# Kernel optimization log

Hardware: AMD Instinct MI355X
Metric: run time of the kernel (lower is better)

The kernel has to match this reference:

```python
import jax, jax.numpy as jnp
import numpy as np

N_ENT, N_REL, E_DIM, R_DIM, K, B = 100000, 64, 128, 128, 32, 16384


def _lookup_maxnorm(table, ids):
    # torch nn.Embedding(max_norm=1): rows with L2 norm > 1 are renormed to 1 at lookup
    x = table[ids]
    n = jnp.linalg.norm(x, axis=-1, keepdims=True)
    return x * jnp.minimum(1.0, 1.0 / jnp.maximum(n, 1e-12))


def setup_inputs() -> dict:
    key = jax.random.key(0)
    ks = jax.random.split(key, 10)
    xavier = lambda k, shp: jax.random.uniform(k, shp, jnp.float32, -1.0, 1.0) * np.sqrt(6.0 / (shp[0] + shp[1]))
    return {
        "idx": jax.random.randint(ks[0], (B,), 0, N_ENT),
        "adj_ent": jax.random.randint(ks[1], (N_ENT, K), 0, N_ENT),
        "adj_rel": jax.random.randint(ks[2], (N_ENT, K), 0, N_REL),
        "ent_table": xavier(ks[3], (N_ENT, E_DIM)),
        "rel_table": xavier(ks[4], (N_REL, R_DIM)),
        "Wr_w": xavier(ks[5], (R_DIM, E_DIM)),
        "Wr_b": jnp.zeros((R_DIM,), jnp.float32),
        "W1_w": xavier(ks[6], (E_DIM, E_DIM)),
        "W1_b": jnp.zeros((E_DIM,), jnp.float32),
        "W2_w": xavier(ks[7], (E_DIM, E_DIM)),
        "W2_b": jnp.zeros((E_DIM,), jnp.float32),
    }


def reference(idx, adj_ent, adj_rel, ent_table, rel_table, Wr_w, Wr_b, W1_w, W1_b, W2_w, W2_b):
    idx = jnp.clip(idx, 0, N_ENT - 1)
    e_ids = adj_ent[idx]                      # [B, K]
    r_ids = adj_rel[idx]                      # [B, K]
    t = _lookup_maxnorm(ent_table, e_ids)     # [B, K, E]
    r = _lookup_maxnorm(rel_table, r_ids)     # [B, K, R]
    h = _lookup_maxnorm(ent_table, idx)       # [B, E]
    # GAT message pass
    hr = h @ Wr_w.T + Wr_b                    # [B, R]
    tr = t @ Wr_w.T + Wr_b                    # [B, K, R]
    score = jnp.sum(jnp.tanh(hr[:, None, :] + r) * tr, axis=-1, keepdims=True)  # [B, K, 1]
    att = jax.nn.softmax(score, axis=1)
    Nh = jnp.sum(t * att, axis=1)             # [B, E]
    # Bi-Interaction aggregate
    leaky = lambda x: jax.nn.leaky_relu(x, 0.2)
    return leaky((h + Nh) @ W1_w.T + W1_b) + leaky((h * Nh) @ W2_w.T + W2_b)
```

## Files before the change

### kernel.cpp

```cpp
#include <hip/hip_runtime.h>
#include <hip/hip_fp16.h>
#include <math.h>

#define N_ENT 100000
#define N_REL 64
#define DIM   128
#define KNB   32
#define BATCH 16384

typedef _Float16 f16;
typedef __attribute__((ext_vector_type(8))) _Float16 f16x8;
typedef __attribute__((ext_vector_type(4))) float floatx4;

__device__ __forceinline__ int clamp_id(int id) {
    return id < 0 ? 0 : (id > N_ENT - 1 ? N_ENT - 1 : id);
}

__device__ __forceinline__ float poly_tanh(float x) {
    const float x2 = x * x;
    return x * fmaf(x2, fmaf(x2, 0.13333334f, -0.33333334f), 1.0f);
}

__global__ __launch_bounds__(256) void k_small(
    const float* __restrict__ Wr, const float* __restrict__ W1,
    const float* __restrict__ W2, f16* __restrict__ Wr16,
    f16* __restrict__ W116, f16* __restrict__ W216,
    const float* __restrict__ rel, __half2* __restrict__ REL2)
{
    if (blockIdx.x < 64) {
        const int t = blockIdx.x * 256 + threadIdx.x;
        Wr16[t] = (f16)Wr[t];
        W116[t] = (f16)W1[t];
        W216[t] = (f16)W2[t];
    } else {
        const int lane = threadIdx.x & 63;
        const int row  = (blockIdx.x - 64) * 4 + (threadIdx.x >> 6);
        const float2 x = *(const float2*)(rel + row * DIM + 2 * lane);
        float ss = x.x * x.x + x.y * x.y;
        #pragma unroll
        for (int m = 1; m < 64; m <<= 1) ss += __shfl_xor(ss, m);
        const float s = fminf(1.0f, 1.0f / fmaxf(sqrtf(ss), 1e-12f));
        REL2[row * 64 + lane] = __floats2half2_rn(x.x * s, x.y * s);
    }
}

__global__ __launch_bounds__(256, 4) void k_pre(
    const float* __restrict__ ent, const f16* __restrict__ B,
    const float* __restrict__ bias, f16* __restrict__ TR16,
    f16* __restrict__ N16)
{
    const int wid  = threadIdx.x >> 6;
    const int lane = threadIdx.x & 63;
    const int strip = blockIdx.x * 4 + wid;
    if (strip >= N_ENT / 16) return;
    const int row0 = strip * 16;
    const int m = lane & 15, quad = lane >> 4;

    const float* __restrict__ src = ent + (size_t)(row0 + m) * DIM + quad * 8;
    float x[4][8];
    #pragma unroll
    for (int kt = 0; kt < 4; ++kt) {
        *(float4*)&x[kt][0] = *(const float4*)(src + kt * 32);
        *(float4*)&x[kt][4] = *(const float4*)(src + kt * 32 + 4);
    }

    float ss = 0.0f;
    #pragma unroll
    for (int kt = 0; kt < 4; ++kt)
        #pragma unroll
        for (int j = 0; j < 8; ++j) ss = fmaf(x[kt][j], x[kt][j], ss);
    ss += __shfl_xor(ss, 16);
    ss += __shfl_xor(ss, 32);
    const float s = fminf(1.0f, 1.0f / fmaxf(sqrtf(ss), 1e-12f));

    f16* __restrict__ ndst = N16 + (size_t)(row0 + m) * DIM + quad * 8;
    f16x8 a[4];
    #pragma unroll
    for (int kt = 0; kt < 4; ++kt) {
        f16x8 av;
        #pragma unroll
        for (int j = 0; j < 8; ++j) av[j] = (f16)(x[kt][j] * s);
        a[kt] = av;
        *(f16x8*)(ndst + kt * 32) = av;
    }

    #pragma unroll
    for (int ct = 0; ct < 8; ++ct) {
        floatx4 acc = {0.0f, 0.0f, 0.0f, 0.0f};
        #pragma unroll
        for (int kt = 0; kt < 4; ++kt) {
            const f16x8 b = *(const f16x8*)(B + (size_t)(ct * 16 + m) * DIM + kt * 32 + quad * 8);
            acc = __builtin_amdgcn_mfma_f32_16x16x32_f16(a[kt], b, acc, 0, 0, 0);
        }
        const float bb = bias[ct * 16 + m];
        #pragma unroll
        for (int r = 0; r < 4; ++r)
            TR16[(size_t)(row0 + quad * 4 + r) * DIM + ct * 16 + m] = (f16)(acc[r] + bb);
    }
}

__global__ __launch_bounds__(256, 4) void k_sa(
    const int* __restrict__ idx, const int* __restrict__ adj_ent,
    const int* __restrict__ adj_rel, const __half2* __restrict__ TR2,
    const __half2* __restrict__ N2, const __half2* __restrict__ REL2,
    __half2* __restrict__ U2, __half2* __restrict__ V2)
{
    const int wid  = threadIdx.x >> 6;
    const int lane = threadIdx.x & 63;
    const int b = blockIdx.x * 4 + wid;

    const int id = clamp_id(idx[b]);
    const float2 hr = __half22float2(TR2[(size_t)id * 64 + lane]);
    const float2 h  = __half22float2(N2[(size_t)id * 64 + lane]);
    const int eL = adj_ent[(size_t)id * KNB + (lane & 31)];
    const int rL = adj_rel[(size_t)id * KNB + (lane & 31)];

    unsigned int tnd[KNB];
    #pragma unroll
    for (int k = 0; k < KNB; ++k) {
        const int e = __builtin_amdgcn_readlane(eL, k);
        tnd[k] = *((const unsigned int*)N2 + (size_t)e * 64 + lane);
    }

    float p[KNB];
    #pragma unroll
    for (int k = 0; k < KNB; ++k) {
        const int e = __builtin_amdgcn_readlane(eL, k);
        const int r = __builtin_amdgcn_readlane(rL, k);
        const float2 tr = __half22float2(TR2[(size_t)e * 64 + lane]);
        const float2 rn = __half22float2(REL2[r * 64 + lane]);
        p[k] = poly_tanh(hr.x + rn.x) * tr.x + poly_tanh(hr.y + rn.y) * tr.y;
    }

    #pragma unroll
    for (int step = 0; step < 5; ++step) {
        const int half = 16 >> step;
        const int mask = 1 << step;
        const bool hi_lane = (lane & mask) != 0;
        #pragma unroll
        for (int i = 0; i < 16; ++i) {
            if (i >= half) break;
            const float lo = p[i], hi = p[i + half];
            const float send = hi_lane ? lo : hi;
            const float recv = __shfl_xor(send, mask);
            p[i] = (hi_lane ? hi : lo) + recv;
        }
    }
    const float sc = p[0] + __shfl_xor(p[0], 32);

    const float ex = __expf(sc);
    float tt = ex;
    #pragma unroll
    for (int m = 1; m < 32; m <<= 1) tt += __shfl_xor(tt, m);
    const float attL = ex * __builtin_amdgcn_rcpf(tt);

    float nh0 = 0.0f, nh1 = 0.0f;
    #pragma unroll
    for (int k = 0; k < KNB; ++k) {
        const float a = __uint_as_float(
            __builtin_amdgcn_readlane(__float_as_uint(attL), k));
        const float2 t = __half22float2(*(const __half2*)&tnd[k]);
        nh0 = fmaf(a, t.x, nh0);
        nh1 = fmaf(a, t.y, nh1);
    }

    U2[(size_t)b * 64 + lane] = __floats2half2_rn(h.x + nh0, h.y + nh1);
    V2[(size_t)b * 64 + lane] = __floats2half2_rn(h.x * nh0, h.y * nh1);
}

__global__ __launch_bounds__(256, 4) void k_gemm_out(
    const f16* __restrict__ U, const f16* __restrict__ V,
    const f16* __restrict__ W1h, const float* __restrict__ b1,
    const f16* __restrict__ W2h, const float* __restrict__ b2,
    float* __restrict__ out)
{
    const int wid  = threadIdx.x >> 6;
    const int lane = threadIdx.x & 63;
    const int g = blockIdx.x * 4 + wid;
    const int strip = g >> 1;
    const int ct0 = (g & 1) * 4;
    const int row0 = strip * 16;
    const int m = lane & 15, quad = lane >> 4;

    f16x8 au[4], av[4];
    #pragma unroll
    for (int kt = 0; kt < 4; ++kt) {
        au[kt] = *(const f16x8*)(U + (size_t)(row0 + m) * DIM + kt * 32 + quad * 8);
        av[kt] = *(const f16x8*)(V + (size_t)(row0 + m) * DIM + kt * 32 + quad * 8);
    }

    #pragma unroll
    for (int c = 0; c < 4; ++c) {
        const int ct = ct0 + c;
        floatx4 accU = {0.0f, 0.0f, 0.0f, 0.0f};
        floatx4 accV = {0.0f, 0.0f, 0.0f, 0.0f};
        #pragma unroll
        for (int kt = 0; kt < 4; ++kt) {
            const f16x8 bu = *(const f16x8*)(W1h + (size_t)(ct * 16 + m) * DIM + kt * 32 + quad * 8);
            const f16x8 bv = *(const f16x8*)(W2h + (size_t)(ct * 16 + m) * DIM + kt * 32 + quad * 8);
            accU = __builtin_amdgcn_mfma_f32_16x16x32_f16(au[kt], bu, accU, 0, 0, 0);
            accV = __builtin_amdgcn_mfma_f32_16x16x32_f16(av[kt], bv, accV, 0, 0, 0);
        }
        const float bb1 = b1[ct * 16 + m];
        const float bb2 = b2[ct * 16 + m];
        #pragma unroll
        for (int r = 0; r < 4; ++r) {
            const float x = accU[r] + bb1;
            const float y = accV[r] + bb2;
            const float lx = x > 0.0f ? x : 0.2f * x;
            const float ly = y > 0.0f ? y : 0.2f * y;
            out[(size_t)(row0 + quad * 4 + r) * DIM + ct * 16 + m] = lx + ly;
        }
    }
}

extern "C" void kernel_launch(void* const* d_in, const int* in_sizes, int n_in,
                              void* d_out, int out_size, void* d_ws, size_t ws_size,
                              hipStream_t stream) {
    (void)in_sizes; (void)n_in; (void)out_size; (void)ws_size;
    const int*   idx     = (const int*)d_in[0];
    const int*   adj_ent = (const int*)d_in[1];
    const int*   adj_rel = (const int*)d_in[2];
    const float* ent     = (const float*)d_in[3];
    const float* rel     = (const float*)d_in[4];
    const float* Wr_w    = (const float*)d_in[5];
    const float* Wr_b    = (const float*)d_in[6];
    const float* W1_w    = (const float*)d_in[7];
    const float* W1_b    = (const float*)d_in[8];
    const float* W2_w    = (const float*)d_in[9];
    const float* W2_b    = (const float*)d_in[10];
    float* out = (float*)d_out;

    char* ws = (char*)d_ws;
    f16* N16   = (f16*)(ws);
    f16* TR16  = (f16*)(ws + 25600000);
    f16* REL16 = (f16*)(ws + 51200000);
    f16* U16   = (f16*)(ws + 51216384);
    f16* V16   = (f16*)(ws + 55410688);
    f16* Wr16  = (f16*)(ws + 59604992);
    f16* W116  = (f16*)(ws + 59637760);
    f16* W216  = (f16*)(ws + 59670528);

    k_small<<<dim3(80), dim3(256), 0, stream>>>(Wr_w, W1_w, W2_w, Wr16, W116, W216,
                                                rel, (__half2*)REL16);
    k_pre<<<dim3((N_ENT / 16 + 3) / 4), dim3(256), 0, stream>>>(ent, Wr16, Wr_b,
                                                                TR16, N16);
    k_sa<<<dim3(BATCH / 4), dim3(256), 0, stream>>>(idx, adj_ent, adj_rel,
                                                    (const __half2*)TR16,
                                                    (const __half2*)N16,
                                                    (const __half2*)REL16,
                                                    (__half2*)U16, (__half2*)V16);
    k_gemm_out<<<dim3(512), dim3(256), 0, stream>>>(U16, V16, W116, W1_b,
                                                    W216, W2_b, out);
}
```

Measured before the change: 195.8 us.

## Interleave projected and normalized entity rows; transpose MFMA operands for vector stores

```diff
diff --git a/kernel.cpp b/kernel.cpp
--- a/kernel.cpp
+++ b/kernel.cpp
@@ -10,6 +10,7 @@
 
 typedef _Float16 f16;
 typedef __attribute__((ext_vector_type(8))) _Float16 f16x8;
+typedef __attribute__((ext_vector_type(4))) _Float16 f16x4;
 typedef __attribute__((ext_vector_type(4))) float floatx4;
 
 __device__ __forceinline__ int clamp_id(int id) {
@@ -46,63 +47,87 @@
 
 __global__ __launch_bounds__(256, 4) void k_pre(
     const float* __restrict__ ent, const f16* __restrict__ B,
-    const float* __restrict__ bias, f16* __restrict__ TR16,
-    f16* __restrict__ N16)
+    const float* __restrict__ bias, f16* __restrict__ C16)
 {
     const int wid  = threadIdx.x >> 6;
     const int lane = threadIdx.x & 63;
-    const int strip = blockIdx.x * 4 + wid;
-    if (strip >= N_ENT / 16) return;
-    const int row0 = strip * 16;
-    const int m = lane & 15, quad = lane >> 4;
-
-    const float* __restrict__ src = ent + (size_t)(row0 + m) * DIM + quad * 8;
-    float x[4][8];
+    const int ds = blockIdx.x * 4 + wid;
+    if (ds >= N_ENT / 32) return;
+    const int row0 = ds * 32;
+    const int mm = lane & 15, quad = lane >> 4;
+
+    const float* __restrict__ src0 = ent + (size_t)(row0 + mm) * DIM + quad * 8;
+    const float* __restrict__ src1 = src0 + 16 * DIM;
+
+    float x0[4][8], x1[4][8];
     #pragma unroll
     for (int kt = 0; kt < 4; ++kt) {
-        *(float4*)&x[kt][0] = *(const float4*)(src + kt * 32);
-        *(float4*)&x[kt][4] = *(const float4*)(src + kt * 32 + 4);
-    }
-
-    float ss = 0.0f;
+        *(float4*)&x0[kt][0] = *(const float4*)(src0 + kt * 32);
+        *(float4*)&x0[kt][4] = *(const float4*)(src0 + kt * 32 + 4);
+        *(float4*)&x1[kt][0] = *(const float4*)(src1 + kt * 32);
+        *(float4*)&x1[kt][4] = *(const float4*)(src1 + kt * 32 + 4);
+    }
+
+    float ss0 = 0.0f, ss1 = 0.0f;
     #pragma unroll
     for (int kt = 0; kt < 4; ++kt)
         #pragma unroll
-        for (int j = 0; j < 8; ++j) ss = fmaf(x[kt][j], x[kt][j], ss);
-    ss += __shfl_xor(ss, 16);
-    ss += __shfl_xor(ss, 32);
-    const float s = fminf(1.0f, 1.0f / fmaxf(sqrtf(ss), 1e-12f));
-
-    f16* __restrict__ ndst = N16 + (size_t)(row0 + m) * DIM + quad * 8;
-    f16x8 a[4];
+        for (int j = 0; j < 8; ++j) {
+            ss0 = fmaf(x0[kt][j], x0[kt][j], ss0);
+            ss1 = fmaf(x1[kt][j], x1[kt][j], ss1);
+        }
+    ss0 += __shfl_xor(ss0, 16); ss0 += __shfl_xor(ss0, 32);
+    ss1 += __shfl_xor(ss1, 16); ss1 += __shfl_xor(ss1, 32);
+    const float s0 = fminf(1.0f, 1.0f / fmaxf(sqrtf(ss0), 1e-12f));
+    const float s1 = fminf(1.0f, 1.0f / fmaxf(sqrtf(ss1), 1e-12f));
+
+    f16* __restrict__ n0 = C16 + (size_t)(row0 + mm) * 256 + 128 + quad * 8;
+    f16* __restrict__ n1 = n0 + 16 * 256;
+    f16x8 a0[4], a1[4];
     #pragma unroll
     for (int kt = 0; kt < 4; ++kt) {
-        f16x8 av;
-        #pragma unroll
-        for (int j = 0; j < 8; ++j) av[j] = (f16)(x[kt][j] * s);
-        a[kt] = av;
-        *(f16x8*)(ndst + kt * 32) = av;
-    }
-
+        f16x8 v0, v1;
+        #pragma unroll
+        for (int j = 0; j < 8; ++j) {
+            v0[j] = (f16)(x0[kt][j] * s0);
+            v1[j] = (f16)(x1[kt][j] * s1);
+        }
+        a0[kt] = v0; a1[kt] = v1;
+        *(f16x8*)(n0 + kt * 32) = v0;
+        *(f16x8*)(n1 + kt * 32) = v1;
+    }
+
+    f16* __restrict__ t0 = C16 + (size_t)(row0 + mm) * 256;
+    f16* __restrict__ t1 = t0 + 16 * 256;
     #pragma unroll
     for (int ct = 0; ct < 8; ++ct) {
-        floatx4 acc = {0.0f, 0.0f, 0.0f, 0.0f};
+        f16x8 w[4];
+        #pragma unroll
+        for (int kt = 0; kt < 4; ++kt)
+            w[kt] = *(const f16x8*)(B + (size_t)(ct * 16 + mm) * DIM + kt * 32 + quad * 8);
+        floatx4 acc0 = {0.0f, 0.0f, 0.0f, 0.0f};
+        floatx4 acc1 = {0.0f, 0.0f, 0.0f, 0.0f};
         #pragma unroll
         for (int kt = 0; kt < 4; ++kt) {
-            const f16x8 b = *(const f16x8*)(B + (size_t)(ct * 16 + m) * DIM + kt * 32 + quad * 8);
-            acc = __builtin_amdgcn_mfma_f32_16x16x32_f16(a[kt], b, acc, 0, 0, 0);
-        }
-        const float bb = bias[ct * 16 + m];
-        #pragma unroll
-        for (int r = 0; r < 4; ++r)
-            TR16[(size_t)(row0 + quad * 4 + r) * DIM + ct * 16 + m] = (f16)(acc[r] + bb);
+            acc0 = __builtin_amdgcn_mfma_f32_16x16x32_f16(w[kt], a0[kt], acc0, 0, 0, 0);
+            acc1 = __builtin_amdgcn_mfma_f32_16x16x32_f16(w[kt], a1[kt], acc1, 0, 0, 0);
+        }
+        const float4 bb = *(const float4*)(bias + ct * 16 + quad * 4);
+        f16x4 o0, o1;
+        #pragma unroll
+        for (int r = 0; r < 4; ++r) {
+            o0[r] = (f16)(acc0[r] + ((const float*)&bb)[r]);
+            o1[r] = (f16)(acc1[r] + ((const float*)&bb)[r]);
+        }
+        *(f16x4*)(t0 + ct * 16 + quad * 4) = o0;
+        *(f16x4*)(t1 + ct * 16 + quad * 4) = o1;
     }
 }
 
 __global__ __launch_bounds__(256, 4) void k_sa(
     const int* __restrict__ idx, const int* __restrict__ adj_ent,
-    const int* __restrict__ adj_rel, const __half2* __restrict__ TR2,
-    const __half2* __restrict__ N2, const __half2* __restrict__ REL2,
+    const int* __restrict__ adj_rel, const unsigned int* __restrict__ C32,
+    const __half2* __restrict__ REL2,
     __half2* __restrict__ U2, __half2* __restrict__ V2)
 {
     const int wid  = threadIdx.x >> 6;
@@ -110,24 +135,26 @@
     const int b = blockIdx.x * 4 + wid;
 
     const int id = clamp_id(idx[b]);
-    const float2 hr = __half22float2(TR2[(size_t)id * 64 + lane]);
-    const float2 h  = __half22float2(N2[(size_t)id * 64 + lane]);
+    const unsigned int hr_u = C32[(size_t)id * 128 + lane];
+    const unsigned int h_u  = C32[(size_t)id * 128 + 64 + lane];
     const int eL = adj_ent[(size_t)id * KNB + (lane & 31)];
     const int rL = adj_rel[(size_t)id * KNB + (lane & 31)];
 
-    unsigned int tnd[KNB];
+    unsigned int trd[KNB], tnd[KNB];
     #pragma unroll
     for (int k = 0; k < KNB; ++k) {
         const int e = __builtin_amdgcn_readlane(eL, k);
-        tnd[k] = *((const unsigned int*)N2 + (size_t)e * 64 + lane);
-    }
-
+        const unsigned int* __restrict__ rowp = C32 + (size_t)e * 128 + lane;
+        trd[k] = rowp[0];
+        tnd[k] = rowp[64];
+    }
+
+    const float2 hr = __half22float2(*(const __half2*)&hr_u);
     float p[KNB];
     #pragma unroll
     for (int k = 0; k < KNB; ++k) {
-        const int e = __builtin_amdgcn_readlane(eL, k);
         const int r = __builtin_amdgcn_readlane(rL, k);
-        const float2 tr = __half22float2(TR2[(size_t)e * 64 + lane]);
+        const float2 tr = __half22float2(*(const __half2*)&trd[k]);
         const float2 rn = __half22float2(REL2[r * 64 + lane]);
         p[k] = poly_tanh(hr.x + rn.x) * tr.x + poly_tanh(hr.y + rn.y) * tr.y;
     }
@@ -164,6 +191,7 @@
         nh1 = fmaf(a, t.y, nh1);
     }
 
+    const float2 h = __half22float2(*(const __half2*)&h_u);
     U2[(size_t)b * 64 + lane] = __floats2half2_rn(h.x + nh0, h.y + nh1);
     V2[(size_t)b * 64 + lane] = __floats2half2_rn(h.x * nh0, h.y * nh1);
 }
@@ -177,40 +205,42 @@
     const int wid  = threadIdx.x >> 6;
     const int lane = threadIdx.x & 63;
     const int g = blockIdx.x * 4 + wid;
-    const int strip = g >> 1;
-    const int ct0 = (g & 1) * 4;
+    const int strip = g >> 2;
+    const int ct0 = (g & 3) * 2;
     const int row0 = strip * 16;
-    const int m = lane & 15, quad = lane >> 4;
+    const int mm = lane & 15, quad = lane >> 4;
 
     f16x8 au[4], av[4];
     #pragma unroll
     for (int kt = 0; kt < 4; ++kt) {
-        au[kt] = *(const f16x8*)(U + (size_t)(row0 + m) * DIM + kt * 32 + quad * 8);
-        av[kt] = *(const f16x8*)(V + (size_t)(row0 + m) * DIM + kt * 32 + quad * 8);
-    }
-
-    #pragma unroll
-    for (int c = 0; c < 4; ++c) {
+        au[kt] = *(const f16x8*)(U + (size_t)(row0 + mm) * DIM + kt * 32 + quad * 8);
+        av[kt] = *(const f16x8*)(V + (size_t)(row0 + mm) * DIM + kt * 32 + quad * 8);
+    }
+
+    #pragma unroll
+    for (int c = 0; c < 2; ++c) {
         const int ct = ct0 + c;
         floatx4 accU = {0.0f, 0.0f, 0.0f, 0.0f};
         floatx4 accV = {0.0f, 0.0f, 0.0f, 0.0f};
         #pragma unroll
         for (int kt = 0; kt < 4; ++kt) {
-            const f16x8 bu = *(const f16x8*)(W1h + (size_t)(ct * 16 + m) * DIM + kt * 32 + quad * 8);
-            const f16x8 bv = *(const f16x8*)(W2h + (size_t)(ct * 16 + m) * DIM + kt * 32 + quad * 8);
-            accU = __builtin_amdgcn_mfma_f32_16x16x32_f16(au[kt], bu, accU, 0, 0, 0);
-            accV = __builtin_amdgcn_mfma_f32_16x16x32_f16(av[kt], bv, accV, 0, 0, 0);
-        }
-        const float bb1 = b1[ct * 16 + m];
-        const float bb2 = b2[ct * 16 + m];
+            const f16x8 wu = *(const f16x8*)(W1h + (size_t)(ct * 16 + mm) * DIM + kt * 32 + quad * 8);
+            const f16x8 wv = *(const f16x8*)(W2h + (size_t)(ct * 16 + mm) * DIM + kt * 32 + quad * 8);
+            accU = __builtin_amdgcn_mfma_f32_16x16x32_f16(wu, au[kt], accU, 0, 0, 0);
+            accV = __builtin_amdgcn_mfma_f32_16x16x32_f16(wv, av[kt], accV, 0, 0, 0);
+        }
+        const float4 bb1 = *(const float4*)(b1 + ct * 16 + quad * 4);
+        const float4 bb2 = *(const float4*)(b2 + ct * 16 + quad * 4);
+        float4 o;
         #pragma unroll
         for (int r = 0; r < 4; ++r) {
-            const float x = accU[r] + bb1;
-            const float y = accV[r] + bb2;
-            const float lx = x > 0.0f ? x : 0.2f * x;
-            const float ly = y > 0.0f ? y : 0.2f * y;
-            out[(size_t)(row0 + quad * 4 + r) * DIM + ct * 16 + m] = lx + ly;
-        }
+            const float xv = accU[r] + ((const float*)&bb1)[r];
+            const float yv = accV[r] + ((const float*)&bb2)[r];
+            const float lx = xv > 0.0f ? xv : 0.2f * xv;
+            const float ly = yv > 0.0f ? yv : 0.2f * yv;
+            ((float*)&o)[r] = lx + ly;
+        }
+        *(float4*)(out + (size_t)(row0 + mm) * DIM + ct * 16 + quad * 4) = o;
     }
 }
 
@@ -232,8 +262,7 @@
     float* out = (float*)d_out;
 
     char* ws = (char*)d_ws;
-    f16* N16   = (f16*)(ws);
-    f16* TR16  = (f16*)(ws + 25600000);
+    f16* C16   = (f16*)(ws);
     f16* REL16 = (f16*)(ws + 51200000);
     f16* U16   = (f16*)(ws + 51216384);
     f16* V16   = (f16*)(ws + 55410688);
@@ -243,13 +272,11 @@
 
     k_small<<<dim3(80), dim3(256), 0, stream>>>(Wr_w, W1_w, W2_w, Wr16, W116, W216,
                                                 rel, (__half2*)REL16);
-    k_pre<<<dim3((N_ENT / 16 + 3) / 4), dim3(256), 0, stream>>>(ent, Wr16, Wr_b,
-                                                                TR16, N16);
+    k_pre<<<dim3((N_ENT / 32 + 3) / 4), dim3(256), 0, stream>>>(ent, Wr16, Wr_b, C16);
     k_sa<<<dim3(BATCH / 4), dim3(256), 0, stream>>>(idx, adj_ent, adj_rel,
-                                                    (const __half2*)TR16,
-                                                    (const __half2*)N16,
+                                                    (const unsigned int*)C16,
                                                     (const __half2*)REL16,
                                                     (__half2*)U16, (__half2*)V16);
-    k_gemm_out<<<dim3(512), dim3(256), 0, stream>>>(U16, V16, W116, W1_b,
-                                                    W216, W2_b, out);
-}
+    k_gemm_out<<<dim3(1024), dim3(256), 0, stream>>>(U16, V16, W116, W1_b,
+                                                     W216, W2_b, out);
+}
```

Result: slower. 206.3 us (+5.4%).
